# Kernel tuning notes

Hardware: AMD Instinct MI355X
Metric: run time of the kernel (lower is better)

The kernel has to match this reference:

```python
import jax, jax.numpy as jnp
import numpy as np

TEMPERATURE = 0.1
EPS = 1e-12

def _l2norm(x):
    # matches F.normalize(x, dim=-1)
    return x / jnp.maximum(jnp.linalg.norm(x, axis=-1, keepdims=True), EPS)

def setup_inputs() -> dict:
    key = jax.random.key(0)
    k1, k2 = jax.random.split(key)
    N, D = 8192, 256
    images = jax.random.normal(k1, (N, D), dtype=jnp.float32)
    captions = jax.random.normal(k2, (N, D), dtype=jnp.float32)
    return {"images": images, "captions": captions}

def reference(images, captions):
    # Batched equivalent of the per-sample loop:
    # for each image i, InfoNCE(anchor=image_i, pos=caption_i, negs=all other captions)
    # and symmetrically for each caption. InfoNCE (unpaired mode) normalizes
    # embeddings, builds logits [pos, negs]/T, and applies CE with target 0.
    # Softmax is permutation-invariant, so this equals symmetric CE on the
    # full NxN similarity matrix with diagonal targets (CLIP loss).
    im = _l2norm(images)    # [N, D]
    cap = _l2norm(captions)  # [N, D]
    logits = jnp.einsum('id,jd->ij', im, cap) / TEMPERATURE  # [N, N]
    diag = jnp.arange(images.shape[0])
    # image->caption losses (rows), caption->image losses (columns)
    loss_i2c = -jax.nn.log_softmax(logits, axis=1)[diag, diag]
    loss_c2i = -jax.nn.log_softmax(logits, axis=0)[diag, diag]
    # original returns mean over the 2N concatenated per-sample losses
    return (jnp.mean(loss_i2c) + jnp.mean(loss_c2i)) * 0.5
```

## Files before the change

kernel.cpp:

```cpp
#include <hip/hip_runtime.h>
#include <hip/hip_bf16.h>
#include <hip/hip_fp8.h>

typedef float f32x4 __attribute__((ext_vector_type(4)));
typedef int i32x4 __attribute__((ext_vector_type(4)));
typedef int i32x8 __attribute__((ext_vector_type(8)));

typedef __attribute__((address_space(3))) void as3_void;
typedef const __attribute__((address_space(1))) void as1_void;

static constexpr int D = 256;
static constexpr float INV_T = 10.0f;

__device__ __forceinline__ unsigned char f2fp8(float x) {
  __hip_fp8_e4m3 q(x);
  return (unsigned char)q.__x;
}

__global__ __launch_bounds__(256) void normalize_kernel(
    const float* __restrict__ im, const float* __restrict__ cap,
    unsigned char* __restrict__ imn, unsigned char* __restrict__ capn,
    float* __restrict__ diag, int N) {
  int tid = blockIdx.x * 256 + threadIdx.x;
  int w = tid >> 6;
  int lane = threadIdx.x & 63;
  if (w >= N) return;
  float4 vi = ((const float4*)(im + (size_t)w * D))[lane];
  float4 vc = ((const float4*)(cap + (size_t)w * D))[lane];
  float ssi = vi.x*vi.x + vi.y*vi.y + vi.z*vi.z + vi.w*vi.w;
  float ssc = vc.x*vc.x + vc.y*vc.y + vc.z*vc.z + vc.w*vc.w;
  #pragma unroll
  for (int m = 1; m < 64; m <<= 1) {
    ssi += __shfl_xor(ssi, m);
    ssc += __shfl_xor(ssc, m);
  }
  float ri = 1.0f / fmaxf(sqrtf(ssi), 1e-12f);
  float rc = 1.0f / fmaxf(sqrtf(ssc), 1e-12f);
  float ax = vi.x*ri, ay = vi.y*ri, az = vi.z*ri, aw = vi.w*ri;
  float cx = vc.x*rc, cy = vc.y*rc, cz = vc.z*rc, cw = vc.w*rc;
  uchar4 ua, uc;
  ua.x = f2fp8(ax); ua.y = f2fp8(ay); ua.z = f2fp8(az); ua.w = f2fp8(aw);
  uc.x = f2fp8(cx); uc.y = f2fp8(cy); uc.z = f2fp8(cz); uc.w = f2fp8(cw);
  ((uchar4*)(imn + (size_t)w * D))[lane] = ua;
  ((uchar4*)(capn + (size_t)w * D))[lane] = uc;
  float d = ax*cx + ay*cy + az*cz + aw*cw;
  #pragma unroll
  for (int m = 1; m < 64; m <<= 1) d += __shfl_xor(d, m);
  if (lane == 0) diag[w] = d * INV_T;
}

__global__ __launch_bounds__(512) void gemm_exp_kernel(
    const unsigned char* __restrict__ A, const unsigned char* __restrict__ Bm,
    float* __restrict__ rowpart, float* __restrict__ colpart, int N) {
  __shared__ unsigned char AsF[65536];
  __shared__ unsigned char BsF[2][32768];
  int bm = blockIdx.x >> 3;
  int grp = blockIdx.x & 7;
  int tid = threadIdx.x;
  int lane = tid & 63;
  int wv = tid >> 6;
  int wm = wv >> 2;
  int wn = wv & 3;
  int rb = lane & 15;
  int kp = lane >> 4;

  f32x4 acc[8][4];

  int sb = wv * 64 + lane;
  int boff[4];
  #pragma unroll
  for (int q = 0; q < 4; ++q) {
    int s = q * 512 + sb;
    int sub = s >> 10, row = (s >> 2) & 255;
    int u = (s & 3) ^ (((row >> 1) + (row >> 3)) & 3);
    boff[q] = row * 256 + sub * 64 + u * 16;
  }

#define VMWAIT(n) asm volatile("s_waitcnt vmcnt(" #n ")" ::: "memory")
#define LGKM0() asm volatile("s_waitcnt lgkmcnt(0)" ::: "memory")
#define BARRIER() asm volatile("s_barrier" ::: "memory")

#define STAGE_B(P, TILE, KH) {                                               \
    const unsigned char* bsrc_ = Bm + (size_t)(TILE) * 65536 + (KH) * 128;   \
    _Pragma("unroll")                                                        \
    for (int q = 0; q < 4; ++q)                                              \
      __builtin_amdgcn_global_load_lds((as1_void*)(bsrc_ + boff[q]),         \
          (as3_void*)(&BsF[P][q * 8192 + wv * 1024]), 16, 0, 0);             \
  }

#define READ_A8(dst, mi, KH) {                                               \
    int row_ = wm * 128 + (mi) * 16 + rb;                                    \
    int h2_ = ((row_ >> 1) + (row_ >> 3)) & 3;                               \
    const unsigned char* ab_ =                                               \
        &AsF[((KH) * 2 + (kp >> 1)) * 16384 + row_ * 64];                    \
    i32x4 lo_ = *(const i32x4*)(ab_ + ((((kp & 1) * 2 + 0) ^ h2_) << 4));    \
    i32x4 hi_ = *(const i32x4*)(ab_ + ((((kp & 1) * 2 + 1) ^ h2_) << 4));    \
    dst = __builtin_shufflevector(lo_, hi_, 0, 1, 2, 3, 4, 5, 6, 7);         \
  }

#define READ_B8(dst, ni, P) {                                                \
    int col_ = wn * 64 + (ni) * 16 + rb;                                     \
    int h2_ = ((col_ >> 1) + (col_ >> 3)) & 3;                               \
    const unsigned char* bb_ = &BsF[P][(kp >> 1) * 16384 + col_ * 64];       \
    i32x4 lo_ = *(const i32x4*)(bb_ + ((((kp & 1) * 2 + 0) ^ h2_) << 4));    \
    i32x4 hi_ = *(const i32x4*)(bb_ + ((((kp & 1) * 2 + 1) ^ h2_) << 4));    \
    dst = __builtin_shufflevector(lo_, hi_, 0, 1, 2, 3, 4, 5, 6, 7);         \
  }

#define COMPUTE(P, KH, CZ) {                                                 \
    i32x8 bfr[4];                                                            \
    READ_B8(bfr[0], 0, P) READ_B8(bfr[1], 1, P)                              \
    READ_B8(bfr[2], 2, P) READ_B8(bfr[3], 3, P)                              \
    _Pragma("unroll")                                                        \
    for (int mi = 0; mi < 8; ++mi) {                                         \
      i32x8 a8;                                                              \
      READ_A8(a8, mi, KH)                                                    \
      __builtin_amdgcn_s_setprio(1);                                         \
      _Pragma("unroll")                                                      \
      for (int ni = 0; ni < 4; ++ni)                                         \
        acc[mi][ni] = __builtin_amdgcn_mfma_scale_f32_16x16x128_f8f6f4(      \
            a8, bfr[ni],                                                     \
            (CZ) ? (f32x4){0.f, 0.f, 0.f, 0.f} : acc[mi][ni],                \
            0, 0, 0, 0x7F7F7F7F, 0, 0x7F7F7F7F);                             \
      __builtin_amdgcn_s_setprio(0);                                         \
    }                                                                        \
    LGKM0();                                                                 \
  }

#define EPILOGUE(BN) {                                                        \
    _Pragma("unroll")                                                         \
    for (int mi = 0; mi < 8; ++mi)                                            \
      _Pragma("unroll")                                                       \
      for (int ni = 0; ni < 4; ++ni)                                          \
        _Pragma("unroll")                                                     \
        for (int r = 0; r < 4; ++r)                                           \
          acc[mi][ni][r] = __expf(acc[mi][ni][r] * INV_T);                    \
    bool sb0 = (lane & 1) != 0, sb1 = (lane & 2) != 0;                        \
    _Pragma("unroll")                                                         \
    for (int mi = 0; mi < 8; ++mi) {                                          \
      float v0 = acc[mi][0][0] + acc[mi][1][0] + acc[mi][2][0] + acc[mi][3][0]; \
      float v1 = acc[mi][0][1] + acc[mi][1][1] + acc[mi][2][1] + acc[mi][3][1]; \
      float v2 = acc[mi][0][2] + acc[mi][1][2] + acc[mi][2][2] + acc[mi][3][2]; \
      float v3 = acc[mi][0][3] + acc[mi][1][3] + acc[mi][2][3] + acc[mi][3][3]; \
      float h0 = (sb0 ? v1 : v0) + __shfl_xor(sb0 ? v0 : v1, 1);              \
      float h1 = (sb0 ? v3 : v2) + __shfl_xor(sb0 ? v2 : v3, 1);              \
      float g  = (sb1 ? h1 : h0) + __shfl_xor(sb1 ? h0 : h1, 2);              \
      g += __shfl_xor(g, 4);                                                  \
      g += __shfl_xor(g, 8);                                                  \
      if ((lane & 12) == 0)                                                   \
        rowpart[(size_t)((BN) * 4 + wn) * N + bm * 256 + wm * 128 + mi * 16 + \
                (lane >> 4) * 4 + (lane & 3)] = g;                            \
    }                                                                         \
    _Pragma("unroll")                                                         \
    for (int ni = 0; ni < 4; ++ni) {                                          \
      float v = 0.f;                                                          \
      _Pragma("unroll")                                                       \
      for (int mi = 0; mi < 8; ++mi)                                          \
        _Pragma("unroll")                                                     \
        for (int r = 0; r < 4; ++r)                                           \
          v += acc[mi][ni][r];                                                \
      v += __shfl_xor(v, 16); v += __shfl_xor(v, 32);                         \
      if (lane < 16)                                                          \
        colpart[(size_t)(bm * 2 + wm) * N + (BN) * 256 + wn * 64 + ni * 16 +  \
                lane] = v;                                                    \
    }                                                                         \
  }

#define TILE(j) (grp * 4 + (j))

  #pragma unroll
  for (int q = 0; q < 8; ++q) {
    int s = q * 512 + sb;
    int sub = s >> 10, row = (s >> 2) & 255;
    int u = (s & 3) ^ (((row >> 1) + (row >> 3)) & 3);
    __builtin_amdgcn_global_load_lds(
        (as1_void*)(A + (size_t)bm * 65536 + row * 256 + sub * 64 + u * 16),
        (as3_void*)(&AsF[q * 8192 + wv * 1024]), 16, 0, 0);
  }
  STAGE_B(0, TILE(0), 0)
  STAGE_B(1, TILE(0), 1)
  VMWAIT(4); BARRIER();

  COMPUTE(0, 0, 1) BARRIER();               STAGE_B(0, TILE(1), 0) VMWAIT(4); BARRIER();
  COMPUTE(1, 1, 0) BARRIER(); EPILOGUE(TILE(0)) STAGE_B(1, TILE(1), 1) VMWAIT(4); BARRIER();
  COMPUTE(0, 0, 1) BARRIER();               STAGE_B(0, TILE(2), 0) VMWAIT(4); BARRIER();
  COMPUTE(1, 1, 0) BARRIER(); EPILOGUE(TILE(1)) STAGE_B(1, TILE(2), 1) VMWAIT(4); BARRIER();
  COMPUTE(0, 0, 1) BARRIER();               STAGE_B(0, TILE(3), 0) VMWAIT(4); BARRIER();
  COMPUTE(1, 1, 0) BARRIER(); EPILOGUE(TILE(2)) STAGE_B(1, TILE(3), 1) VMWAIT(4); BARRIER();
  COMPUTE(0, 0, 1) BARRIER();               VMWAIT(0); BARRIER();
  COMPUTE(1, 1, 0) EPILOGUE(TILE(3))
  VMWAIT(0);

#undef TILE
#undef EPILOGUE
#undef COMPUTE
#undef READ_B8
#undef READ_A8
#undef STAGE_B
#undef VMWAIT
#undef LGKM0
#undef BARRIER
}

__global__ __launch_bounds__(256) void reduce_kernel(
    const float* __restrict__ rowpart, const float* __restrict__ colpart,
    const float* __restrict__ diag, float* __restrict__ out,
    int N, int NPr, int NPc) {
  __shared__ float redr[4][64], redc[4][64];
  int w = threadIdx.x >> 6, s = threadIdx.x & 63;
  int i = blockIdx.x * 64 + s;
  float rs = 0.f, cs = 0.f;
  for (int k = w; k < NPr; k += 4) rs += rowpart[(size_t)k * N + i];
  for (int k = w; k < NPc; k += 4) cs += colpart[(size_t)k * N + i];
  redr[w][s] = rs; redc[w][s] = cs;
  __syncthreads();
  if (w == 0) {
    float R = redr[0][s] + redr[1][s] + redr[2][s] + redr[3][s];
    float C = redc[0][s] + redc[1][s] + redc[2][s] + redc[3][s];
    float l = logf(R) + logf(C) - 2.0f * diag[i];
    #pragma unroll
    for (int m = 1; m < 64; m <<= 1) l += __shfl_xor(l, m);
    if (s == 0) atomicAdd(out, l * (0.5f / (float)N));
  }
}

extern "C" void kernel_launch(void* const* d_in, const int* in_sizes, int n_in,
                              void* d_out, int out_size, void* d_ws, size_t ws_size,
                              hipStream_t stream) {
  const float* images = (const float*)d_in[0];
  const float* captions = (const float*)d_in[1];
  int N = in_sizes[0] / D;
  int NPr = 128;
  int NPc = 64;
  char* w = (char*)d_ws;
  size_t off = 0;
  unsigned char* imn  = (unsigned char*)(w + off); off += (size_t)N * D;
  unsigned char* capn = (unsigned char*)(w + off); off += (size_t)N * D;
  float* diag    = (float*)(w + off); off += (size_t)N * 4;
  float* rowpart = (float*)(w + off); off += (size_t)NPr * N * 4;
  float* colpart = (float*)(w + off); off += (size_t)NPc * N * 4;
  float* out = (float*)d_out;

  normalize_kernel<<<N / 4, 256, 0, stream>>>(images, captions, imn, capn, diag, N);
  gemm_exp_kernel<<<256, 512, 0, stream>>>(imn, capn, rowpart, colpart, N);
  hipMemsetAsync(out, 0, sizeof(float), stream);
  reduce_kernel<<<N / 64, 256, 0, stream>>>(rowpart, colpart, diag, out, N, NPr, NPc);
}
```

Before: 63.69 us.

## Add sub-block term to LDS swizzle and reorder MFMA loop to B-outer

Adds the K sub-block index to the XOR swizzle used for both the A and B LDS tiles, applied consistently at the global-to-LDS staging and at the fragment reads, to spread bank accesses across sub-blocks. The compute loop is also inverted so each B fragment is read once and A fragments are re-read from LDS inside the inner loop, rather than holding four B fragments in registers. This lowers register pressure but reads A from LDS four times as often, which may raise LDS traffic and latency.

New measurement: 88.13 us. 1.38x slower.

```diff
diff --git a/kernel.cpp b/kernel.cpp
--- a/kernel.cpp
+++ b/kernel.cpp
@@ -72,7 +72,7 @@
   for (int q = 0; q < 4; ++q) {
     int s = q * 512 + sb;
     int sub = s >> 10, row = (s >> 2) & 255;
-    int u = (s & 3) ^ (((row >> 1) + (row >> 3)) & 3);
+    int u = (s & 3) ^ (((row >> 1) + (row >> 3) + sub) & 3);
     boff[q] = row * 256 + sub * 64 + u * 16;
   }
 
@@ -90,38 +90,39 @@
 
 #define READ_A8(dst, mi, KH) {                                               \
     int row_ = wm * 128 + (mi) * 16 + rb;                                    \
-    int h2_ = ((row_ >> 1) + (row_ >> 3)) & 3;                               \
-    const unsigned char* ab_ =                                               \
-        &AsF[((KH) * 2 + (kp >> 1)) * 16384 + row_ * 64];                    \
-    i32x4 lo_ = *(const i32x4*)(ab_ + ((((kp & 1) * 2 + 0) ^ h2_) << 4));    \
-    i32x4 hi_ = *(const i32x4*)(ab_ + ((((kp & 1) * 2 + 1) ^ h2_) << 4));    \
+    int sub_ = (KH) * 2 + (kp >> 1);                                         \
+    int h3_ = ((row_ >> 1) + (row_ >> 3) + sub_) & 3;                        \
+    const unsigned char* ab_ = &AsF[sub_ * 16384 + row_ * 64];               \
+    i32x4 lo_ = *(const i32x4*)(ab_ + ((((kp & 1) * 2 + 0) ^ h3_) << 4));    \
+    i32x4 hi_ = *(const i32x4*)(ab_ + ((((kp & 1) * 2 + 1) ^ h3_) << 4));    \
     dst = __builtin_shufflevector(lo_, hi_, 0, 1, 2, 3, 4, 5, 6, 7);         \
   }
 
 #define READ_B8(dst, ni, P) {                                                \
     int col_ = wn * 64 + (ni) * 16 + rb;                                     \
-    int h2_ = ((col_ >> 1) + (col_ >> 3)) & 3;                               \
-    const unsigned char* bb_ = &BsF[P][(kp >> 1) * 16384 + col_ * 64];       \
-    i32x4 lo_ = *(const i32x4*)(bb_ + ((((kp & 1) * 2 + 0) ^ h2_) << 4));    \
-    i32x4 hi_ = *(const i32x4*)(bb_ + ((((kp & 1) * 2 + 1) ^ h2_) << 4));    \
+    int sub_ = kp >> 1;                                                      \
+    int h3_ = ((col_ >> 1) + (col_ >> 3) + sub_) & 3;                        \
+    const unsigned char* bb_ = &BsF[P][sub_ * 16384 + col_ * 64];            \
+    i32x4 lo_ = *(const i32x4*)(bb_ + ((((kp & 1) * 2 + 0) ^ h3_) << 4));    \
+    i32x4 hi_ = *(const i32x4*)(bb_ + ((((kp & 1) * 2 + 1) ^ h3_) << 4));    \
     dst = __builtin_shufflevector(lo_, hi_, 0, 1, 2, 3, 4, 5, 6, 7);         \
   }
 
 #define COMPUTE(P, KH, CZ) {                                                 \
-    i32x8 bfr[4];                                                            \
-    READ_B8(bfr[0], 0, P) READ_B8(bfr[1], 1, P)                              \
-    READ_B8(bfr[2], 2, P) READ_B8(bfr[3], 3, P)                              \
     _Pragma("unroll")                                                        \
-    for (int mi = 0; mi < 8; ++mi) {                                         \
-      i32x8 a8;                                                              \
-      READ_A8(a8, mi, KH)                                                    \
+    for (int ni = 0; ni < 4; ++ni) {                                         \
+      i32x8 b8;                                                              \
+      READ_B8(b8, ni, P)                                                     \
       __builtin_amdgcn_s_setprio(1);                                         \
       _Pragma("unroll")                                                      \
-      for (int ni = 0; ni < 4; ++ni)                                         \
+      for (int mi = 0; mi < 8; ++mi) {                                       \
+        i32x8 a8;                                                            \
+        READ_A8(a8, mi, KH)                                                  \
         acc[mi][ni] = __builtin_amdgcn_mfma_scale_f32_16x16x128_f8f6f4(      \
-            a8, bfr[ni],                                                     \
+            a8, b8,                                                          \
             (CZ) ? (f32x4){0.f, 0.f, 0.f, 0.f} : acc[mi][ni],                \
             0, 0, 0, 0x7F7F7F7F, 0, 0x7F7F7F7F);                             \
+      }                                                                      \
       __builtin_amdgcn_s_setprio(0);                                         \
     }                                                                        \
     LGKM0();                                                                 \
@@ -172,7 +173,7 @@
   for (int q = 0; q < 8; ++q) {
     int s = q * 512 + sb;
     int sub = s >> 10, row = (s >> 2) & 255;
-    int u = (s & 3) ^ (((row >> 1) + (row >> 3)) & 3);
+    int u = (s & 3) ^ (((row >> 1) + (row >> 3) + sub) & 3);
     __builtin_amdgcn_global_load_lds(
         (as1_void*)(A + (size_t)bm * 65536 + row * 256 + sub * 64 + u * 16),
         (as3_void*)(&AsF[q * 8192 + wv * 1024]), 16, 0, 0);
```
